# Performance work log

Hardware: AMD Instinct MI355X
Metric: run time of the kernel (lower is better)

Reference implementation:

```python
import jax, jax.numpy as jnp
import numpy as np

N = 131072          # collocation points per dataset
C_WAVE = 1.0        # wave speed c
DIMS = [2, 256, 256, 256, 256, 1]


def _glorot(k, shape):
    fan_in, fan_out = shape
    std = jnp.sqrt(2.0 / (fan_in + fan_out)).astype(jnp.float32)
    return std * jax.random.normal(k, shape, dtype=jnp.float32)


def setup_inputs() -> dict:
    key = jax.random.key(0)
    ks = jax.random.split(key, 16)
    inp = {}
    for i in range(5):
        inp[f"W{i}"] = _glorot(ks[i], (DIMS[i], DIMS[i + 1]))
        inp[f"b{i}"] = jnp.zeros((DIMS[i + 1],), jnp.float32)
    inp["tx_equation"] = jax.random.uniform(ks[10], (N, 2), dtype=jnp.float32)
    inp["tx_init"] = jax.random.uniform(ks[11], (N, 2), dtype=jnp.float32)
    # initial condition points have t=0 in practice; values don't affect the math pattern
    inp["tx_init"] = inp["tx_init"].at[:, 0].set(0.0)
    inp["tx_bound"] = jax.random.uniform(ks[12], (N, 2), dtype=jnp.float32)
    return inp


def _mlp(params, tx):
    # tanh MLP: (..., 2) -> (..., 1)
    h = tx
    for W, b in params[:-1]:
        h = jnp.tanh(h @ W + b)
    W, b = params[-1]
    return h @ W + b


def reference(W0, b0, W1, b1, W2, b2, W3, b3, W4, b4,
              tx_equation, tx_init, tx_bound):
    params = [(W0, b0), (W1, b1), (W2, b2), (W3, b3), (W4, b4)]

    def u_scalar(tx):  # tx: (2,) -> scalar u(t, x)
        return _mlp(params, tx[None, :])[0, 0]

    # PDE residual: u_tt - c^2 * u_xx via per-point Hessian diagonal (input_diagonal_hessian)
    hess = jax.vmap(jax.hessian(u_scalar))(tx_equation)      # (N, 2, 2)
    u_tt = hess[:, 0, 0]
    u_xx = hess[:, 1, 1]
    pde_residual = (u_tt - (C_WAVE ** 2) * u_xx)[:, None]     # (N, 1)

    # Initial conditions: u and du/dt (input_gradient)
    u_init, g = jax.vmap(jax.value_and_grad(u_scalar))(tx_init)  # (N,), (N, 2)
    u_phi = u_init[:, None]                                   # (N, 1)
    du_dt_psi = g[:, 0][:, None]                              # (N, 1)

    # Boundary: plain forward
    u_bound = _mlp(params, tx_bound)                          # (N, 1)

    return jnp.stack([pde_residual, u_phi, du_dt_psi, u_bound], axis=0)  # (4, N, 1)
```

## Files before the change

kernel.cpp:

```cpp
#include <hip/hip_runtime.h>
#include <math.h>

#define N_PTS 131072
#define HID   256

typedef __attribute__((ext_vector_type(8)))  _Float16 f16x8;
typedef __attribute__((ext_vector_type(4)))  float    f32x4;
typedef __attribute__((ext_vector_type(16))) float    f32x16;
typedef unsigned int u32;
typedef __attribute__((address_space(1))) const u32 gu32;
typedef __attribute__((address_space(3))) u32       lu32;

#define LDS_HI  0
#define LDS_W   65536
#define LDS_SZ  131072

__device__ __forceinline__ int act_off(int row, int kbyte) {
    return row * 512 + (kbyte ^ ((row & 7) << 4));
}
__device__ __forceinline__ int w_off64(int n, int kg) {
    return n * 128 + ((kg ^ (n & 7)) << 4);
}
__device__ __forceinline__ void tanh_f1(float z, float& h, float& f1) {
    float zc = fminf(fmaxf(z, -15.0f), 15.0f);
    float s  = __expf(2.0f * zc);
    float r  = __builtin_amdgcn_rcpf(s + 1.0f);
    h  = fmaf(-2.0f, r, 1.0f);
    f1 = 4.0f * s * r * r;
}

__global__ void prep_w(const float* __restrict__ W1, const float* __restrict__ W2,
                       const float* __restrict__ W3, char* __restrict__ ws)
{
    int idx = blockIdx.x * 256 + threadIdx.x;
    int l = idx >> 16;
    int e = idx & 65535;
    int k = e >> 8, n = e & 255;
    const float* W = (l == 0) ? W1 : (l == 1) ? W2 : W3;
    float w = W[e];
    int period = k >> 6;
    int kk = k & 63;
    int byte_in = w_off64(n, kk >> 3) + (kk & 7) * 2;
    char* base = ws + (size_t)(l * 4 + period) * 32768;
    *(_Float16*)(base + byte_in) = (_Float16)w;
}

template<int S, int PTS>
__global__ void __launch_bounds__(512, 1)
pinn_mfma(const float* __restrict__ W0, const float* __restrict__ b0,
          const float* __restrict__ b1, const float* __restrict__ b2,
          const float* __restrict__ b3,
          const float* __restrict__ W4, const float* __restrict__ b4,
          const char* __restrict__ wpre,
          const float* __restrict__ tx, float* __restrict__ out)
{
    extern __shared__ char lds[];
    const int tid  = threadIdx.x;
    const int lane = tid & 63;
    const int wid  = tid >> 6;
    const int wr   = wid & 1;
    const int wc   = wid >> 1;
    const int pbase = blockIdx.x * PTS;
    constexpr int CG = 512 / PTS;
    constexpr int NC = 256 / CG;
    const int ep  = tid / CG;
    const int ec0 = (tid % CG) * NC;

    {
        const char* src = wpre;
        char* dst = lds + LDS_W;
        #pragma unroll
        for (int q = 0; q < 4; ++q) {
            int o = (wid * 4 + q) * 1024;
            __builtin_amdgcn_global_load_lds((gu32*)(src + o + lane * 16),
                                             (lu32*)(dst + o), 16, 0, 0);
        }
    }

    {
        const float tt = tx[2 * (pbase + ep) + 0];
        const float xx = tx[2 * (pbase + ep) + 1];
        for (int cb = ec0; cb < ec0 + NC; cb += 8) {
            alignas(16) float w0r[8], w1r[8], bb[8];
            *(f32x4*)&w0r[0] = *(const f32x4*)(W0 + cb);
            *(f32x4*)&w0r[4] = *(const f32x4*)(W0 + cb + 4);
            *(f32x4*)&w1r[0] = *(const f32x4*)(W0 + HID + cb);
            *(f32x4*)&w1r[4] = *(const f32x4*)(W0 + HID + cb + 4);
            *(f32x4*)&bb[0]  = *(const f32x4*)(b0 + cb);
            *(f32x4*)&bb[4]  = *(const f32x4*)(b0 + cb + 4);
            f16x8 vhi[S];
            #pragma unroll
            for (int j = 0; j < 8; ++j) {
                float z = fmaf(tt, w0r[j], fmaf(xx, w1r[j], bb[j]));
                float h, f1;
                tanh_f1(z, h, f1);
                vhi[0][j] = (_Float16)h;
                if (S == 2) {
                    vhi[1][j] = (_Float16)(f1 * w0r[j]);
                } else if (S == 4) {
                    float d1 = w0r[j] + w1r[j];
                    float d2 = w0r[j] - w1r[j];
                    float f2 = -2.0f * h * f1;
                    vhi[1][j] = (_Float16)(f1 * d1);
                    vhi[2][j] = (_Float16)(f1 * d2);
                    vhi[3][j] = (_Float16)(f2 * d1 * d2);
                }
            }
            #pragma unroll
            for (int s2 = 0; s2 < S; ++s2) {
                int row = ep * S + s2;
                *(f16x8*)(lds + LDS_HI + act_off(row, cb * 2)) = vhi[s2];
            }
        }
    }

    const int c0 = (wc * 2) * 32 + (lane & 31);
    float bcv[3][2];
    bcv[0][0] = b1[c0]; bcv[0][1] = b1[c0 + 32];
    bcv[1][0] = b2[c0]; bcv[1][1] = b2[c0 + 32];
    bcv[2][0] = b3[c0]; bcv[2][1] = b3[c0 + 32];

    asm volatile("s_waitcnt lgkmcnt(0)" ::: "memory");
    __builtin_amdgcn_sched_barrier(0);

    #pragma unroll
    for (int l = 0; l < 3; ++l) {
        f32x16 acc[2][2];
        #pragma unroll
        for (int i = 0; i < 2; ++i)
            #pragma unroll
            for (int j = 0; j < 2; ++j)
                acc[i][j] = (f32x16){0.f,0.f,0.f,0.f,0.f,0.f,0.f,0.f,
                                     0.f,0.f,0.f,0.f,0.f,0.f,0.f,0.f};

        #pragma unroll
        for (int ph = 0; ph < 4; ++ph) {
            const int g = l * 4 + ph;
            __builtin_amdgcn_s_barrier();
            if (g < 11) {
                const char* src = wpre + (size_t)(g + 1) * 32768;
                char* dst = lds + LDS_W + ((g + 1) & 1) * 32768;
                #pragma unroll
                for (int q = 0; q < 4; ++q) {
                    int o = (wid * 4 + q) * 1024;
                    __builtin_amdgcn_global_load_lds((gu32*)(src + o + lane * 16),
                                                     (lu32*)(dst + o), 16, 0, 0);
                }
                asm volatile("s_waitcnt vmcnt(4)" ::: "memory");
            } else {
                asm volatile("s_waitcnt vmcnt(0)" ::: "memory");
            }
            __builtin_amdgcn_sched_barrier(0);

            const char* wb = lds + LDS_W + (g & 1) * 32768;
            #pragma unroll
            for (int ks = 0; ks < 4; ++ks) {
                const int kb = ph * 128 + ks * 32 + ((lane >> 5) << 4);
                const int kg = ks * 2 + (lane >> 5);
                f16x8 av[2], bv[2];
                #pragma unroll
                for (int i = 0; i < 2; ++i) {
                    const int row = (wr * 2 + i) * 32 + (lane & 31);
                    av[i] = *(const f16x8*)(lds + LDS_HI + act_off(row, kb));
                }
                #pragma unroll
                for (int j = 0; j < 2; ++j) {
                    const int n = (wc * 2 + j) * 32 + (lane & 31);
                    bv[j] = *(const f16x8*)(wb + w_off64(n, kg));
                }
                __builtin_amdgcn_s_setprio(1);
                acc[0][0] = __builtin_amdgcn_mfma_f32_32x32x16_f16(av[0], bv[0], acc[0][0], 0, 0, 0);
                acc[0][1] = __builtin_amdgcn_mfma_f32_32x32x16_f16(av[0], bv[1], acc[0][1], 0, 0, 0);
                acc[1][0] = __builtin_amdgcn_mfma_f32_32x32x16_f16(av[1], bv[0], acc[1][0], 0, 0, 0);
                acc[1][1] = __builtin_amdgcn_mfma_f32_32x32x16_f16(av[1], bv[1], acc[1][1], 0, 0, 0);
                __builtin_amdgcn_s_setprio(0);
            }
        }
        __builtin_amdgcn_s_barrier();

        #pragma unroll
        for (int i = 0; i < 2; ++i) {
            #pragma unroll
            for (int j = 0; j < 2; ++j) {
                const int colj = (wc * 2 + j) * 32 + (lane & 31);
                const float bias = bcv[l][j];
                const int rtb = (wr * 2 + i) * 32 + 4 * (lane >> 5);
                #pragma unroll
                for (int q = 0; q < 4; ++q) {
                    const int rb = rtb + 8 * q;
                    if (S == 4) {
                        float z0 = acc[i][j][4*q+0] + bias;
                        float z1 = acc[i][j][4*q+1];
                        float z2 = acc[i][j][4*q+2];
                        float zm = acc[i][j][4*q+3];
                        float h, f1;
                        tanh_f1(z0, h, f1);
                        float f2 = -2.0f * h * f1;
                        *(_Float16*)(lds + LDS_HI + act_off(rb+0, colj*2)) = (_Float16)h;
                        *(_Float16*)(lds + LDS_HI + act_off(rb+1, colj*2)) = (_Float16)(f1 * z1);
                        *(_Float16*)(lds + LDS_HI + act_off(rb+2, colj*2)) = (_Float16)(f1 * z2);
                        *(_Float16*)(lds + LDS_HI + act_off(rb+3, colj*2)) =
                            (_Float16)(fmaf(f1, zm, f2 * z1 * z2));
                    } else if (S == 2) {
                        #pragma unroll
                        for (int pp = 0; pp < 2; ++pp) {
                            float z0 = acc[i][j][4*q+2*pp+0] + bias;
                            float zd = acc[i][j][4*q+2*pp+1];
                            float h, f1;
                            tanh_f1(z0, h, f1);
                            *(_Float16*)(lds + LDS_HI + act_off(rb+2*pp+0, colj*2)) = (_Float16)h;
                            *(_Float16*)(lds + LDS_HI + act_off(rb+2*pp+1, colj*2)) = (_Float16)(f1 * zd);
                        }
                    } else {
                        #pragma unroll
                        for (int m = 0; m < 4; ++m) {
                            float z0 = acc[i][j][4*q+m] + bias;
                            float h, f1;
                            tanh_f1(z0, h, f1);
                            *(_Float16*)(lds + LDS_HI + act_off(rb+m, colj*2)) = (_Float16)h;
                        }
                    }
                }
            }
        }
        asm volatile("s_waitcnt lgkmcnt(0)" ::: "memory");
        __builtin_amdgcn_sched_barrier(0);
    }
    __builtin_amdgcn_s_barrier();

    if (S == 4) {
        const int p   = tid >> 4;
        const int seg = tid & 15;
        const int k0  = seg * 16;
        const int row = 4 * p + 3;
        float d = 0.0f;
        #pragma unroll
        for (int kb = 0; kb < 16; kb += 8) {
            f16x8 h8 = *(const f16x8*)(lds + LDS_HI + act_off(row, (k0 + kb) * 2));
            alignas(16) float wv[8];
            *(f32x4*)&wv[0] = *(const f32x4*)(W4 + k0 + kb);
            *(f32x4*)&wv[4] = *(const f32x4*)(W4 + k0 + kb + 4);
            #pragma unroll
            for (int j = 0; j < 8; ++j) d = fmaf((float)h8[j], wv[j], d);
        }
        #pragma unroll
        for (int off = 8; off > 0; off >>= 1) d += __shfl_down(d, off, 16);
        if (seg == 0) out[0 * N_PTS + pbase + p] = d;
    } else {
        const int row = tid >> 2;
        const int seg = tid & 3;
        const int k0  = seg * 64;
        float d = 0.0f;
        #pragma unroll
        for (int kb = 0; kb < 64; kb += 8) {
            f16x8 h8 = *(const f16x8*)(lds + LDS_HI + act_off(row, (k0 + kb) * 2));
            alignas(16) float wv[8];
            *(f32x4*)&wv[0] = *(const f32x4*)(W4 + k0 + kb);
            *(f32x4*)&wv[4] = *(const f32x4*)(W4 + k0 + kb + 4);
            #pragma unroll
            for (int j = 0; j < 8; ++j) d = fmaf((float)h8[j], wv[j], d);
        }
        d += __shfl_down(d, 2, 4);
        d += __shfl_down(d, 1, 4);
        if (seg == 0) {
            if (S == 2) {
                const int p = row >> 1;
                if ((row & 1) == 0) out[1 * N_PTS + pbase + p] = d + b4[0];
                else                out[2 * N_PTS + pbase + p] = d;
            } else {
                out[3 * N_PTS + pbase + row] = d + b4[0];
            }
        }
    }
}

extern "C" void kernel_launch(void* const* d_in, const int* in_sizes, int n_in,
                              void* d_out, int out_size, void* d_ws, size_t ws_size,
                              hipStream_t stream) {
    const float* W0 = (const float*)d_in[0];
    const float* b0 = (const float*)d_in[1];
    const float* W1 = (const float*)d_in[2];
    const float* b1 = (const float*)d_in[3];
    const float* W2 = (const float*)d_in[4];
    const float* b2 = (const float*)d_in[5];
    const float* W3 = (const float*)d_in[6];
    const float* b3 = (const float*)d_in[7];
    const float* W4 = (const float*)d_in[8];
    const float* b4 = (const float*)d_in[9];
    const float* tx_eq    = (const float*)d_in[10];
    const float* tx_init  = (const float*)d_in[11];
    const float* tx_bound = (const float*)d_in[12];
    float* out = (float*)d_out;
    char* wpre = (char*)d_ws;

    hipFuncSetAttribute((const void*)pinn_mfma<4,32>,  hipFuncAttributeMaxDynamicSharedMemorySize, LDS_SZ);
    hipFuncSetAttribute((const void*)pinn_mfma<2,64>,  hipFuncAttributeMaxDynamicSharedMemorySize, LDS_SZ);
    hipFuncSetAttribute((const void*)pinn_mfma<1,128>, hipFuncAttributeMaxDynamicSharedMemorySize, LDS_SZ);

    prep_w<<<768, 256, 0, stream>>>(W1, W2, W3, wpre);
    pinn_mfma<4,32> <<<N_PTS/32,  512, LDS_SZ, stream>>>(W0,b0,b1,b2,b3,W4,b4,wpre,tx_eq,   out);
    pinn_mfma<2,64> <<<N_PTS/64,  512, LDS_SZ, stream>>>(W0,b0,b1,b2,b3,W4,b4,wpre,tx_init, out);
    pinn_mfma<1,128><<<N_PTS/128, 512, LDS_SZ, stream>>>(W0,b0,b1,b2,b3,W4,b4,wpre,tx_bound,out);
}
```

Before: 646.0 us.

## Shrink weight staging to 8KB slabs to allow multiple blocks per CU

Re-tiles the staged fp16 weights from 32KB K-periods into 8KB slabs of 16 K-rows, each double-buffered in LDS, which cuts LDS use from 128KB to 80KB and raises launch bounds to allow several blocks per CU. The inner loop becomes 16 small phases per layer, each with a barrier and a full vmcnt wait. Inter-block occupancy is meant to hide latency in place of deep intra-block prefetch. The tanh derivative is also simplified to 1-h^2 and the input clamp is removed, which risks overflow to inf in exp for large inputs (rcp then gives h=1, so it is probably safe). Syncs at layer boundaries are adjusted to match.

```diff
diff --git a/kernel.cpp b/kernel.cpp
--- a/kernel.cpp
+++ b/kernel.cpp
@@ -13,20 +13,16 @@
 
 #define LDS_HI  0
 #define LDS_W   65536
-#define LDS_SZ  131072
+#define LDS_SZ  81920
 
 __device__ __forceinline__ int act_off(int row, int kbyte) {
     return row * 512 + (kbyte ^ ((row & 7) << 4));
 }
-__device__ __forceinline__ int w_off64(int n, int kg) {
-    return n * 128 + ((kg ^ (n & 7)) << 4);
-}
 __device__ __forceinline__ void tanh_f1(float z, float& h, float& f1) {
-    float zc = fminf(fmaxf(z, -15.0f), 15.0f);
-    float s  = __expf(2.0f * zc);
-    float r  = __builtin_amdgcn_rcpf(s + 1.0f);
+    float s = __expf(2.0f * z);
+    float r = __builtin_amdgcn_rcpf(s + 1.0f);
     h  = fmaf(-2.0f, r, 1.0f);
-    f1 = 4.0f * s * r * r;
+    f1 = (1.0f - h) * (1.0f + h);
 }
 
 __global__ void prep_w(const float* __restrict__ W1, const float* __restrict__ W2,
@@ -38,15 +34,13 @@
     int k = e >> 8, n = e & 255;
     const float* W = (l == 0) ? W1 : (l == 1) ? W2 : W3;
     float w = W[e];
-    int period = k >> 6;
-    int kk = k & 63;
-    int byte_in = w_off64(n, kk >> 3) + (kk & 7) * 2;
-    char* base = ws + (size_t)(l * 4 + period) * 32768;
-    *(_Float16*)(base + byte_in) = (_Float16)w;
+    int slab = l * 16 + (k >> 4);
+    int byte_in = ((k >> 3) & 1) * 4096 + n * 16 + (k & 7) * 2;
+    *(_Float16*)(ws + (size_t)slab * 8192 + byte_in) = (_Float16)w;
 }
 
 template<int S, int PTS>
-__global__ void __launch_bounds__(512, 1)
+__global__ void __launch_bounds__(512, 4)
 pinn_mfma(const float* __restrict__ W0, const float* __restrict__ b0,
           const float* __restrict__ b1, const float* __restrict__ b2,
           const float* __restrict__ b3,
@@ -66,16 +60,8 @@
     const int ep  = tid / CG;
     const int ec0 = (tid % CG) * NC;
 
-    {
-        const char* src = wpre;
-        char* dst = lds + LDS_W;
-        #pragma unroll
-        for (int q = 0; q < 4; ++q) {
-            int o = (wid * 4 + q) * 1024;
-            __builtin_amdgcn_global_load_lds((gu32*)(src + o + lane * 16),
-                                             (lu32*)(dst + o), 16, 0, 0);
-        }
-    }
+    __builtin_amdgcn_global_load_lds((gu32*)(wpre + tid * 16),
+                                     (lu32*)(lds + LDS_W + tid * 16), 16, 0, 0);
 
     {
         const float tt = tx[2 * (pbase + ep) + 0];
@@ -120,7 +106,9 @@
     bcv[1][0] = b2[c0]; bcv[1][1] = b2[c0 + 32];
     bcv[2][0] = b3[c0]; bcv[2][1] = b3[c0 + 32];
 
-    asm volatile("s_waitcnt lgkmcnt(0)" ::: "memory");
+    asm volatile("s_waitcnt vmcnt(0) lgkmcnt(0)" ::: "memory");
+    __builtin_amdgcn_sched_barrier(0);
+    __builtin_amdgcn_s_barrier();
     __builtin_amdgcn_sched_barrier(0);
 
     #pragma unroll
@@ -134,47 +122,37 @@
                                      0.f,0.f,0.f,0.f,0.f,0.f,0.f,0.f};
 
         #pragma unroll
-        for (int ph = 0; ph < 4; ++ph) {
-            const int g = l * 4 + ph;
-            __builtin_amdgcn_s_barrier();
-            if (g < 11) {
-                const char* src = wpre + (size_t)(g + 1) * 32768;
-                char* dst = lds + LDS_W + ((g + 1) & 1) * 32768;
-                #pragma unroll
-                for (int q = 0; q < 4; ++q) {
-                    int o = (wid * 4 + q) * 1024;
-                    __builtin_amdgcn_global_load_lds((gu32*)(src + o + lane * 16),
-                                                     (lu32*)(dst + o), 16, 0, 0);
-                }
-                asm volatile("s_waitcnt vmcnt(4)" ::: "memory");
-            } else {
+        for (int ph = 0; ph < 16; ++ph) {
+            const int g = l * 16 + ph;
+            if (ph > 0) {
                 asm volatile("s_waitcnt vmcnt(0)" ::: "memory");
-            }
-            __builtin_amdgcn_sched_barrier(0);
-
-            const char* wb = lds + LDS_W + (g & 1) * 32768;
-            #pragma unroll
-            for (int ks = 0; ks < 4; ++ks) {
-                const int kb = ph * 128 + ks * 32 + ((lane >> 5) << 4);
-                const int kg = ks * 2 + (lane >> 5);
-                f16x8 av[2], bv[2];
-                #pragma unroll
-                for (int i = 0; i < 2; ++i) {
-                    const int row = (wr * 2 + i) * 32 + (lane & 31);
-                    av[i] = *(const f16x8*)(lds + LDS_HI + act_off(row, kb));
-                }
-                #pragma unroll
-                for (int j = 0; j < 2; ++j) {
-                    const int n = (wc * 2 + j) * 32 + (lane & 31);
-                    bv[j] = *(const f16x8*)(wb + w_off64(n, kg));
-                }
-                __builtin_amdgcn_s_setprio(1);
-                acc[0][0] = __builtin_amdgcn_mfma_f32_32x32x16_f16(av[0], bv[0], acc[0][0], 0, 0, 0);
-                acc[0][1] = __builtin_amdgcn_mfma_f32_32x32x16_f16(av[0], bv[1], acc[0][1], 0, 0, 0);
-                acc[1][0] = __builtin_amdgcn_mfma_f32_32x32x16_f16(av[1], bv[0], acc[1][0], 0, 0, 0);
-                acc[1][1] = __builtin_amdgcn_mfma_f32_32x32x16_f16(av[1], bv[1], acc[1][1], 0, 0, 0);
-                __builtin_amdgcn_s_setprio(0);
-            }
+                __builtin_amdgcn_s_barrier();
+                __builtin_amdgcn_sched_barrier(0);
+            }
+            if (g < 47) {
+                __builtin_amdgcn_global_load_lds(
+                    (gu32*)(wpre + (size_t)(g + 1) * 8192 + tid * 16),
+                    (lu32*)(lds + LDS_W + ((g + 1) & 1) * 8192 + tid * 16), 16, 0, 0);
+            }
+            const int kbyte = ph * 32 + ((lane >> 5) << 4);
+            f16x8 av[2], bv[2];
+            #pragma unroll
+            for (int i = 0; i < 2; ++i) {
+                const int row = (wr * 2 + i) * 32 + (lane & 31);
+                av[i] = *(const f16x8*)(lds + LDS_HI + act_off(row, kbyte));
+            }
+            const char* wb = lds + LDS_W + (g & 1) * 8192 + ((lane >> 5) << 12);
+            #pragma unroll
+            for (int j = 0; j < 2; ++j) {
+                const int n = (wc * 2 + j) * 32 + (lane & 31);
+                bv[j] = *(const f16x8*)(wb + n * 16);
+            }
+            __builtin_amdgcn_s_setprio(1);
+            acc[0][0] = __builtin_amdgcn_mfma_f32_32x32x16_f16(av[0], bv[0], acc[0][0], 0, 0, 0);
+            acc[0][1] = __builtin_amdgcn_mfma_f32_32x32x16_f16(av[0], bv[1], acc[0][1], 0, 0, 0);
+            acc[1][0] = __builtin_amdgcn_mfma_f32_32x32x16_f16(av[1], bv[0], acc[1][0], 0, 0, 0);
+            acc[1][1] = __builtin_amdgcn_mfma_f32_32x32x16_f16(av[1], bv[1], acc[1][1], 0, 0, 0);
+            __builtin_amdgcn_s_setprio(0);
         }
         __builtin_amdgcn_s_barrier();
 
@@ -223,10 +201,11 @@
                 }
             }
         }
-        asm volatile("s_waitcnt lgkmcnt(0)" ::: "memory");
+        asm volatile("s_waitcnt vmcnt(0) lgkmcnt(0)" ::: "memory");
+        __builtin_amdgcn_sched_barrier(0);
+        __builtin_amdgcn_s_barrier();
         __builtin_amdgcn_sched_barrier(0);
     }
-    __builtin_amdgcn_s_barrier();
 
     if (S == 4) {
         const int p   = tid >> 4;
```

Measured after the change: 685.0 us. 6.0% more time.
